# Kernel optimization log

Hardware: AMD Instinct MI355X
Metric: run time of the kernel (lower is better)

Reference implementation:

```python
import jax, jax.numpy as jnp
import numpy as np

# ---------------- irreps metadata: list of (mul, l, parity) ----------------
IR_A  = [(1, 0, 1)]                                        # '0e' input scalars
IR_B  = [(10,0,1),(10,0,-1),(10,0,1),(5,1,1),(5,1,-1)]     # Gate input, dim 60
IR_C  = [(10,0,1),(10,0,-1),(5,1,1),(5,1,-1)]              # Gate output, dim 50
IR_D  = [(1,0,-1),(6,0,1)]                                 # '0o + 6x0e', dim 7
IR_SH = [(1,0,1),(1,1,-1)]                                 # '0e + 1o'
CONVS = [(IR_A,IR_B),(IR_C,IR_B),(IR_C,IR_B),(IR_C,IR_B),(IR_C,IR_D)]
R_BASIS  = 2
DIAMETER = 5.0   # source used 1.5 -> degenerate 1^3 kernel; enlarged to exercise the steerable conv
STEP     = 1.0

def irdim(ir):
    return sum(m*(2*l+1) for m,l,_ in ir)

def irslices(ir):
    out, o = [], 0
    for m,l,_ in ir:
        d = m*(2*l+1); out.append(slice(o,o+d)); o += d
    return out

# normalized Clebsch-Gordan (wigner3j * sqrt(2*l_out+1)) for l<=1
_eps = np.zeros((3,3,3))
for a,b,c in [(0,1,2),(1,2,0),(2,0,1)]:
    _eps[a,b,c] = 1.0; _eps[b,a,c] = -1.0
CG = {
    (0,0,0): np.ones((1,1,1)),
    (0,1,1): np.eye(3).reshape(1,3,3),
    (1,0,1): np.eye(3).reshape(3,1,3),
    (1,1,0): (np.eye(3)/np.sqrt(3.0)).reshape(3,3,1),
    (1,1,1): _eps/np.sqrt(2.0),
}

def tp_ins(ir1, iro):
    ins = []
    for i1,(m1,l1,p1) in enumerate(ir1):
        for i2,(m2,l2,p2) in enumerate(IR_SH):
            for io,(mo,lo,po) in enumerate(iro):
                if po == p1*p2 and abs(l1-l2) <= lo <= l1+l2:
                    ins.append((i1,i2,io))
    return ins

def tp_numel(ir1, iro):
    return sum(R_BASIS*ir1[i1][0]*IR_SH[i2][0]*iro[io][0] for i1,i2,io in tp_ins(ir1,iro))

def lin_ins(ir1, iro):
    return [(i,j) for i,(m1,l1,p1) in enumerate(ir1)
                  for j,(m2,l2,p2) in enumerate(iro) if l1==l2 and p1==p2]

def lin_numel(ir1, iro):
    return sum(ir1[i][0]*iro[j][0] for i,j in lin_ins(ir1,iro))

def _lattice_features():
    # lattice offsets, smooth_finite radial basis (with cutoff) and SH ('0e+1o', component norm)
    r = DIAMETER/2.0
    s = int(np.floor(r/STEP))
    c = np.arange(-s, s+1, dtype=np.float64)*STEP
    lat = np.stack(np.meshgrid(c, c, c, indexing='ij'), -1)            # [K,K,K,3]
    d = np.linalg.norm(lat, axis=-1)
    vals = np.linspace(0.0, r, R_BASIS+2)[1:-1]
    step = vals[1]-vals[0]
    diff = (d[...,None]-vals)/step
    sus = lambda t: np.where(t>0, np.exp(-1.0/np.where(t>0, t, 1.0)), 0.0)
    emb = 1.14136*np.exp(2.0)*sus(diff+1.0)*sus(1.0-diff)              # [K,K,K,R]
    unit = lat/np.maximum(d, 1e-9)[...,None]
    sh = np.concatenate([np.ones_like(d)[...,None],
                         np.sqrt(3.0)*unit[...,[1,2,0]]], -1)          # [K,K,K,4], e3nn (y,z,x) order
    return jnp.asarray(emb, jnp.float32), jnp.asarray(sh, jnp.float32)

EMB, SH = _lattice_features()

def build_kernel(ir_in, ir_out, tw, lw):
    sin, sout, ssh = irslices(ir_in), irslices(ir_out), irslices(IR_SH)
    K = EMB.shape[0]
    k = jnp.zeros((K, K, K, irdim(ir_in), irdim(ir_out)), jnp.float32)
    off = 0
    for i1,i2,io in tp_ins(ir_in, ir_out):
        m1,l1,_ = ir_in[i1]; m2,l2,_ = IR_SH[i2]; mo,lo,_ = ir_out[io]
        n = R_BASIS*m1*m2*mo
        w = tw[off:off+n].reshape(R_BASIS, m1, mo); off += n           # m2 == 1 for SH
        cg = jnp.asarray(CG[(l1,l2,lo)], jnp.float32)
        alpha = 1.0/np.sqrt(m1*m2*R_BASIS)
        shseg = SH[..., ssh[i2]]                                       # [K,K,K,2l2+1]
        blk = alpha*jnp.einsum('xyzr,ruw,xyzj,ijk->xyzuiwk', EMB, w, shseg, cg)
        k = k.at[:,:,:, sin[i1], sout[io]].add(
            blk.reshape(K, K, K, m1*(2*l1+1), mo*(2*lo+1)))
    # self-connection Linear at the kernel center (radial basis vanishes at r=0)
    M = jnp.zeros((irdim(ir_in), irdim(ir_out)), jnp.float32)
    off = 0
    for i,j in lin_ins(ir_in, ir_out):
        m1,l1,_ = ir_in[i]; mo,_,_ = ir_out[j]
        w = lw[off:off+m1*mo].reshape(m1, mo); off += m1*mo
        eye = jnp.eye(2*l1+1, dtype=jnp.float32)
        blk = (1.0/np.sqrt(m1))*jnp.einsum('uw,ik->uiwk', w, eye)
        M = M.at[sin[i], sout[j]].add(blk.reshape(m1*(2*l1+1), mo*(2*l1+1)))
    cc = K//2
    return k.at[cc, cc, cc].set(M)

def equiv_conv(x, k):
    return jax.lax.conv_general_dilated(x, k, (1,1,1), 'SAME',
        dimension_numbers=('NXYZC', 'XYZIO', 'NXYZC'))

def gate(y):
    # Gate('10x0e+10x0o', [gelu, tanh], '10x0e', [sigmoid], '5x1e+5x1o')
    s = jnp.concatenate([jax.nn.gelu(y[..., :10]), jnp.tanh(y[..., 10:20])], -1)
    g = jax.nn.sigmoid(y[..., 20:30])                                  # 10 gate scalars
    v = y[..., 30:60].reshape(y.shape[:-1]+(10,3))*g[..., None]        # gate 5x1e + 5x1o
    return jnp.concatenate([s, v.reshape(y.shape[:-1]+(30,))], -1)

def _forward(x, tws, lws):
    y = x
    for i,(a,b) in enumerate(CONVS):
        y = equiv_conv(y, build_kernel(a, b, tws[i], lws[i]))
        if i < len(CONVS)-1:
            y = gate(y)
    return jnp.sum(y, axis=(1, 2, 3))                                  # [B, 7]

def setup_inputs() -> dict:
    key = jax.random.key(0)
    ks = jax.random.split(key, 11)
    inp = {'x': jax.random.normal(ks[0], (2, 48, 48, 48, 1), jnp.float32)}
    for i,(a,b) in enumerate(CONVS):
        inp[f'tp_w{i}'] = jax.random.normal(ks[1+i], (tp_numel(a,b),), jnp.float32)
        inp[f'lin_w{i}'] = jax.random.normal(ks[6+i], (lin_numel(a,b),), jnp.float32)
    return inp

def reference(x, tp_w0, tp_w1, tp_w2, tp_w3, tp_w4,
              lin_w0, lin_w1, lin_w2, lin_w3, lin_w4):
    return _forward(x, [tp_w0, tp_w1, tp_w2, tp_w3, tp_w4],
                    [lin_w0, lin_w1, lin_w2, lin_w3, lin_w4])
```

## Files before the change

kernel.cpp:

```cpp
#include <hip/hip_runtime.h>
#include <hip/hip_bf16.h>
#include <math.h>


typedef __attribute__((ext_vector_type(8))) short bf16x8;
typedef __attribute__((ext_vector_type(4))) float f32x4;
typedef __attribute__((ext_vector_type(4))) unsigned int u32x4;

struct TpPath { int off, ci, co, m1, l1, i2, mo, lo; float alpha; };
struct LinPath { int off, ci, co, m1, l, mo; float norm; };

__device__ __constant__ TpPath g_tp[19] = {
  {0,  0,  0, 1, 0, 0, 10, 0, 0.70710678f},
  {20, 0, 20, 1, 0, 0, 10, 0, 0.70710678f},
  {40, 0, 45, 1, 0, 1,  5, 1, 0.70710678f},
  {0,    0,  0, 10, 0, 0, 10, 0, 0.22360680f},
  {200,  0, 20, 10, 0, 0, 10, 0, 0.22360680f},
  {400,  0, 45, 10, 0, 1,  5, 1, 0.22360680f},
  {500, 10, 10, 10, 0, 0, 10, 0, 0.22360680f},
  {700, 10, 30, 10, 0, 1,  5, 1, 0.22360680f},
  {800, 20, 30,  5, 1, 0,  5, 1, 0.31622777f},
  {850, 20, 10,  5, 1, 1, 10, 0, 0.31622777f},
  {950, 20, 45,  5, 1, 1,  5, 1, 0.31622777f},
  {1000,35, 45,  5, 1, 0,  5, 1, 0.31622777f},
  {1050,35,  0,  5, 1, 1, 10, 0, 0.31622777f},
  {1150,35, 20,  5, 1, 1, 10, 0, 0.31622777f},
  {1250,35, 30,  5, 1, 1,  5, 1, 0.31622777f},
  {0,    0, 1, 10, 0, 0, 6, 0, 0.22360680f},
  {120, 10, 0, 10, 0, 0, 1, 0, 0.22360680f},
  {140, 20, 0,  5, 1, 1, 1, 0, 0.31622777f},
  {150, 35, 1,  5, 1, 1, 6, 0, 0.31622777f},
};

__device__ __constant__ LinPath g_lin[9] = {
  {0,  0,  0, 1, 0, 10, 1.0f},
  {10, 0, 20, 1, 0, 10, 1.0f},
  {0,   0,  0, 10, 0, 10, 0.31622777f},
  {100, 0, 20, 10, 0, 10, 0.31622777f},
  {200,10, 10, 10, 0, 10, 0.31622777f},
  {300,20, 30,  5, 1,  5, 0.44721360f},
  {325,35, 45,  5, 1,  5, 0.44721360f},
  {0,  0, 1, 10, 0, 6, 0.31622777f},
  {60,10, 0, 10, 0, 1, 0.31622777f},
};

__device__ inline float sus_f(float t) { return t > 0.f ? __expf(-1.f / t) : 0.f; }

__global__ void build_tp_kernel(const float* __restrict__ tw, float* __restrict__ kbuf,
                                int CIN, int COUT, int path_base) {
  TpPath p = g_tp[path_base + blockIdx.x];
  const int dl1 = 2 * p.l1 + 1, dlo = 2 * p.lo + 1;
  const int du = p.m1 * dl1, dw = p.mo * dlo;
  const int total = 125 * du * dw;
  const float C0 = 1.14136f * expf(2.0f);
  for (int e = threadIdx.x; e < total; e += blockDim.x) {
    int xyz = e / (du * dw);
    int rem = e % (du * dw);
    int ui = rem / dw, wk = rem % dw;
    int u = ui / dl1, i = ui % dl1;
    int w = wk / dlo, kk = wk % dlo;
    int kx = xyz / 25, ky = (xyz / 5) % 5, kz = xyz % 5;
    float cx = (float)(kx - 2), cy = (float)(ky - 2), cz = (float)(kz - 2);
    float d = sqrtf(cx * cx + cy * cy + cz * cz);
    float t = 1.2f * d;
    float e0 = C0 * sus_f(t) * sus_f(2.f - t);
    float e1 = C0 * sus_f(t - 1.f) * sus_f(3.f - t);
    float radial = e0 * tw[p.off + (0 * p.m1 + u) * p.mo + w] +
                   e1 * tw[p.off + (1 * p.m1 + u) * p.mo + w];
    float invd = (d > 0.f) ? 1.f / d : 0.f;
    const float s3 = 1.7320508f;
    float sh1[3] = { s3 * cy * invd, s3 * cz * invd, s3 * cx * invd };
    float shfac;
    if (p.l1 == 0 && p.i2 == 0)      shfac = 1.f;
    else if (p.l1 == 0)              shfac = sh1[kk];
    else if (p.i2 == 0)              shfac = (i == kk) ? 1.f : 0.f;
    else if (p.lo == 0)              shfac = sh1[i] * 0.57735027f;
    else {
      if (i == kk) shfac = 0.f;
      else {
        int j = 3 - i - kk;
        float sgn = (j == (i + 1) % 3) ? 1.f : -1.f;
        shfac = sgn * sh1[j] * 0.70710678f;
      }
    }
    kbuf[(size_t)(xyz * CIN + p.ci + ui) * COUT + p.co + wk] = p.alpha * radial * shfac;
  }
}

__global__ void set_center_kernel(const float* __restrict__ lw, float* __restrict__ kbuf,
                                  int CIN, int COUT, int lin_base, int nlin) {
  for (int l = 0; l < nlin; l++) {
    LinPath q = g_lin[lin_base + l];
    int dl = 2 * q.l + 1;
    int tot = q.m1 * q.mo * dl;
    for (int e = threadIdx.x; e < tot; e += blockDim.x) {
      int u = e / (q.mo * dl);
      int r = e % (q.mo * dl);
      int w = r / dl, ii = r % dl;
      kbuf[(size_t)(62 * CIN + q.ci + u * dl + ii) * COUT + q.co + w * dl + ii] =
          q.norm * lw[q.off + u * q.mo + w];
    }
  }
}

__global__ void convert_w(const float* __restrict__ kbuf, unsigned short* __restrict__ kwbT,
                          int CIN, int COUT) {
  int idx = blockIdx.x * 256 + threadIdx.x;
  if (idx >= 125 * 64 * 64) return;
  int tap = idx >> 12, co = (idx >> 6) & 63, ci = idx & 63;
  float v = (ci < CIN && co < COUT) ? kbuf[((size_t)tap * CIN + ci) * COUT + co] : 0.f;
  __hip_bfloat16 h = __float2bfloat16(v);
  kwbT[idx] = *(unsigned short*)&h;
}

__global__ void build_w0(const float* __restrict__ k0, unsigned short* __restrict__ wb0L) {
  int idx = blockIdx.x * 256 + threadIdx.x;
  if (idx >= 5 * 2 * 64 * 32) return;
  int k = idx & 31, co = (idx >> 5) & 63, mf = (idx >> 11) & 1, dxi = idx >> 12;
  float v = 0.f;
  if (co < 60) {
    if (mf == 0) {
      int dy = k >> 3, dz = k & 7;
      if (dz < 5) v = k0[(size_t)(((dxi * 5 + dy) * 5 + dz)) * 60 + co];
    } else {
      int kg = k >> 3, dz = k & 7;
      if (kg == 0 && dz < 5) v = k0[(size_t)(((dxi * 5 + 4) * 5 + dz)) * 60 + co];
    }
  }
  __hip_bfloat16 h = __float2bfloat16(v);
  wb0L[idx] = *(unsigned short*)&h;
}

__device__ inline float gelu_f(float x) {
  float inner = 0.79788456f * (x + 0.044715f * x * x * x);
  return 0.5f * x * (1.f + tanhf(inner));
}
__device__ inline float sigm_f(float x) { return 1.f / (1.f + __expf(-x)); }

__device__ inline int eidx(int c, int z) {
  return c * 16 + ((((z >> 2) ^ (c & 3)) << 2) | (z & 3));
}
__device__ inline int oidx(int z, int p) { return z * 32 + (p ^ z); }
__device__ inline int uidx(int e) {
  return (e & ~31) | ((e & 31) ^ ((e >> 5) & 15));
}

__device__ inline void gate_tile(const float* my, unsigned int* myO, int z) {
#pragma unroll
  for (int p = 0; p < 25; p++) {
    float a0, a1;
    if (p < 5) {
      a0 = gelu_f(my[eidx(2 * p, z)]);
      a1 = gelu_f(my[eidx(2 * p + 1, z)]);
    } else if (p < 10) {
      a0 = tanhf(my[eidx(2 * p, z)]);
      a1 = tanhf(my[eidx(2 * p + 1, z)]);
    } else {
      int q0 = 2 * (p - 10), q1 = q0 + 1;
      a0 = my[eidx(30 + q0, z)] * sigm_f(my[eidx(20 + q0 / 3, z)]);
      a1 = my[eidx(30 + q1, z)] * sigm_f(my[eidx(20 + q1 / 3, z)]);
    }
    __hip_bfloat162 p2;
    p2.x = __float2bfloat16(a0);
    p2.y = __float2bfloat16(a1);
    myO[oidx(z, p)] = *(unsigned int*)&p2;
  }
#pragma unroll
  for (int p = 25; p < 32; p++) myO[oidx(z, p)] = 0u;
}

template <int NT>
__device__ inline void epilogue_gate(f32x4 (&acc)[3][NT], float* my,
                                     unsigned short* out_, int n, int x, int y,
                                     int l, int lm, int kg) {
  unsigned int* myO = (unsigned int*)(my + 1024);
#pragma unroll
  for (int zt = 0; zt < 3; zt++) {
#pragma unroll
    for (int nt = 0; nt < NT; nt++)
      *(f32x4*)(my + (lm + 16 * nt) * 16 + ((kg ^ (lm & 3)) << 2)) = acc[zt][nt];
    if (l < 16) gate_tile(my, myO, l);
    unsigned int* gout = (unsigned int*)out_ +
        ((size_t)(((n * 48 + x) * 48 + y) * 48 + 16 * zt)) * 32;
#pragma unroll 1
    for (int e = l; e < 512; e += 64) gout[e] = myO[uidx(e)];
  }
}

template <int CIN, int COUT, int MODE>
__global__ __launch_bounds__(512, 2)
void conv_mfma(const unsigned short* __restrict__ act, const short* __restrict__ kwbT,
               void* __restrict__ out_) {
  constexpr int NTH = (MODE == 0) ? 2 : 1;
  constexpr int KC = (CIN + 31) / 32;
  __shared__ __align__(16) unsigned int Albs[12 * 48 * 32];

  const int tid = threadIdx.x;
  const int l = tid & 63;
  const int w = tid >> 6;
  const int wp = w & 3;
  const int ch = w >> 2;
  const int lm = l & 15;
  const int kg = l >> 4;
  const int co_off = (MODE == 0) ? ch * 32 : 0;

  const int bid = blockIdx.x;
  const int yb = bid % 6;
  const int x = (bid / 6) % 48;
  const int n = bid / (6 * 48);

  int g_off[9]; bool g_ok[9]; int l_off[9];
#pragma unroll
  for (int i = 0; i < 9; i++) {
    int e = tid + i * 512;
    int yi = e / 384;
    int rem = e % 384;
    int zin = rem >> 3, u = rem & 7;
    int yin = 8 * yb + yi - 2;
    g_ok[i] = (yin >= 0) && (yin < 48);
    int yc = min(max(yin, 0), 47);
    g_off[i] = (yc * 48 + zin) * 64 + u * 8;
    l_off[i] = (yi * 48 + zin) * 32 + ((u ^ (zin & 7)) << 2);
  }

  f32x4 acc[2][3][NTH];
#pragma unroll
  for (int yy = 0; yy < 2; yy++)
#pragma unroll
    for (int zt = 0; zt < 3; zt++)
#pragma unroll
      for (int nt = 0; nt < NTH; nt++) acc[yy][zt][nt] = (f32x4){0.f, 0.f, 0.f, 0.f};

  u32x4 rg[9];
  const int xlo = max(x - 2, 0), xhi = min(x + 2, 47);

#define LOADP(xin_)                                                            \
  {                                                                            \
    const unsigned short* pb = act + (size_t)((n * 48 + (xin_)) * 2304) * 64;  \
    _Pragma("unroll")                                                          \
    for (int i = 0; i < 9; i++)                                                \
      rg[i] = g_ok[i] ? *(const u32x4*)(pb + g_off[i])                         \
                      : (u32x4){0u, 0u, 0u, 0u};                               \
  }

  LOADP(xlo);
#pragma unroll 1
  for (int xin = xlo; xin <= xhi; ++xin) {
    __syncthreads();
#pragma unroll
    for (int i = 0; i < 9; i++)
      *(u32x4*)((unsigned int*)Albs + l_off[i]) = rg[i];
    __syncthreads();
    if (xin < xhi) LOADP(xin + 1);

    if (MODE == 0 || w < 4) {
      const int dxi = xin - x + 2;
      const short* Albs_s = (const short*)Albs;
#pragma unroll 1
      for (int dy = 0; dy < 5; dy++) {
        const int tapbase = (dxi * 5 + dy) * 5;
#pragma unroll
        for (int dz = 0; dz < 5; dz++) {
          bf16x8 bfr[NTH * KC];
          {
            const short* wb_ = kwbT + ((size_t)(tapbase + dz) << 12) +
                               (co_off + lm) * 64 + kg * 8;
#pragma unroll
            for (int nt = 0; nt < NTH; nt++)
#pragma unroll
              for (int kc = 0; kc < KC; kc++)
                bfr[nt * KC + kc] = *(const bf16x8*)(wb_ + nt * 1024 + kc * 32);
          }
          bf16x8 afr[2][3][KC];
#pragma unroll
          for (int zt = 0; zt < 3; zt++) {
            const int zraw = 16 * zt + lm + dz - 2;
            const int zc = min(max(zraw, 0), 47);
            const bool zval = (zraw >= 0) && (zraw < 48);
#pragma unroll
            for (int yy = 0; yy < 2; yy++) {
              const int yrow = 2 * wp + yy + dy;
              const int rowoff = (yrow * 48 + zc) * 64;
#pragma unroll
              for (int kc = 0; kc < KC; kc++) {
                int u = (4 * kc + kg) ^ (zc & 7);
                bf16x8 v = *(const bf16x8*)(Albs_s + rowoff + u * 8);
                afr[yy][zt][kc] = zval ? v : (bf16x8)(short)0;
              }
            }
          }
#pragma unroll
          for (int yy = 0; yy < 2; yy++)
#pragma unroll
            for (int zt = 0; zt < 3; zt++)
#pragma unroll
              for (int nt = 0; nt < NTH; nt++)
#pragma unroll
                for (int kc = 0; kc < KC; kc++)
                  acc[yy][zt][nt] = __builtin_amdgcn_mfma_f32_16x16x32_bf16(
                      afr[yy][zt][kc], bfr[nt * KC + kc], acc[yy][zt][nt], 0, 0, 0);
        }
      }
    }
  }
#undef LOADP

  if constexpr (MODE == 0) {
    __syncthreads();
    float* base = (float*)Albs;
    int par = 0;
#pragma unroll
    for (int yy = 0; yy < 2; yy++) {
#pragma unroll
      for (int zt = 0; zt < 3; zt++) {
        float* my = base + par * 6144 + wp * 1536;
        unsigned int* myO = (unsigned int*)(my + 1024);
#pragma unroll
        for (int nt = 0; nt < NTH; nt++)
          *(f32x4*)(my + (co_off + lm + 16 * nt) * 16 + ((kg ^ (lm & 3)) << 2)) =
              acc[yy][zt][nt];
        __syncthreads();
        if (ch == 0 && l < 16) gate_tile(my, myO, l);
        __syncthreads();
        unsigned int* gout = (unsigned int*)out_ +
            ((size_t)(((n * 48 + x) * 48 + (8 * yb + 2 * wp + yy)) * 48 + 16 * zt)) * 32;
#pragma unroll
        for (int q = 0; q < 4; q++) {
          int e = ch * 256 + q * 64 + l;
          gout[e] = myO[uidx(e)];
        }
        par ^= 1;
      }
    }
  } else {
    if (w < 4) {
      float s = 0.f;
#pragma unroll
      for (int yy = 0; yy < 2; yy++)
#pragma unroll
        for (int zt = 0; zt < 3; zt++)
#pragma unroll
          for (int r = 0; r < 4; r++) s += acc[yy][zt][0][r];
      s += __shfl_xor(s, 16);
      s += __shfl_xor(s, 32);
      if (l < 7) atomicAdd(&((float*)out_)[n * 7 + l], s);
    }
  }
}

__global__ __launch_bounds__(256, 4)
void conv0_mfma(const float* __restrict__ in_, const short* __restrict__ wb0L,
                unsigned short* __restrict__ out_) {
  __shared__ float A0[8 * 72];
  __shared__ __align__(16) float outbuf0[4 * 1536];

  const int tid = threadIdx.x;
  const int l = tid & 63;
  const int w = tid >> 6;
  const int lm = l & 15;
  const int kg = l >> 4;
  const int yb = blockIdx.x % 12;
  const int x = (blockIdx.x / 12) % 48;
  const int n = blockIdx.x / (12 * 48);

  f32x4 acc[3][4];
#pragma unroll
  for (int zt = 0; zt < 3; zt++)
#pragma unroll
    for (int nt = 0; nt < 4; nt++) acc[zt][nt] = (f32x4){0.f, 0.f, 0.f, 0.f};

  for (int dxi = 0; dxi < 5; dxi++) {
    int xin = x + dxi - 2;
    if (xin < 0 || xin >= 48) continue;
    __syncthreads();
    for (int e = tid; e < 8 * 72; e += 256) {
      int yi = e / 72, zz = e % 72;
      int yin = 4 * yb + yi - 2, zin = zz - 2;
      A0[e] = (yin >= 0 && yin < 48 && zin >= 0 && zin < 48)
                  ? in_[(size_t)((n * 48 + xin) * 48 + yin) * 48 + zin] : 0.f;
    }
    __syncthreads();
#pragma unroll
    for (int mf = 0; mf < 2; mf++) {
      const short* wbp = wb0L + ((size_t)(dxi * 2 + mf) * 64 + lm) * 32 + kg * 8;
      bf16x8 bfr[4];
#pragma unroll
      for (int nt = 0; nt < 4; nt++) bfr[nt] = *(const bf16x8*)(wbp + nt * 16 * 32);
      const int row = mf ? (w + 4) : (w + kg);
#pragma unroll
      for (int zt = 0; zt < 3; zt++) {
        const float* ap = A0 + row * 72 + 16 * zt + lm;
        union { bf16x8 v; unsigned short s[8]; } af;
#pragma unroll
        for (int j = 0; j < 8; j++) {
          __hip_bfloat16 h = __float2bfloat16(ap[j]);
          af.s[j] = *(unsigned short*)&h;
        }
#pragma unroll
        for (int nt = 0; nt < 4; nt++)
          acc[zt][nt] = __builtin_amdgcn_mfma_f32_16x16x32_bf16(
              af.v, bfr[nt], acc[zt][nt], 0, 0, 0);
      }
    }
  }

  float* my = outbuf0 + w * 1536;
  epilogue_gate<4>(acc, my, out_, n, x, 4 * yb + w, l, lm, kg);
}

extern "C" void kernel_launch(void* const* d_in, const int* in_sizes, int n_in,
                              void* d_out, int out_size, void* d_ws, size_t ws_size,
                              hipStream_t stream) {
  const float* x   = (const float*)d_in[0];
  const float* tw0 = (const float*)d_in[1];
  const float* lw0 = (const float*)d_in[2];
  const float* tw1 = (const float*)d_in[3];
  const float* lw1 = (const float*)d_in[4];
  const float* tw2 = (const float*)d_in[5];
  const float* lw2 = (const float*)d_in[6];
  const float* tw3 = (const float*)d_in[7];
  const float* lw3 = (const float*)d_in[8];
  const float* tw4 = (const float*)d_in[9];
  const float* lw4 = (const float*)d_in[10];

  float* ws = (float*)d_ws;
  float* k0 = ws;
  float* k1 = k0 + 7500;
  float* k2 = k1 + 375000;
  float* k3 = k2 + 375000;
  float* k4 = k3 + 375000;
  unsigned short* actA = (unsigned short*)(ws + 1200000);
  unsigned short* actB = actA + 14155776;
  unsigned short* wb1 = (unsigned short*)(ws + 15360000);
  unsigned short* wb2 = wb1 + 512000;
  unsigned short* wb3 = wb2 + 512000;
  unsigned short* wb4 = wb3 + 512000;
  unsigned short* wb0L = wb4 + 512000;

  hipMemsetAsync(ws, 0, (size_t)1176250 * sizeof(float), stream);
  hipMemsetAsync(d_out, 0, (size_t)out_size * sizeof(float), stream);

  build_tp_kernel<<<3, 128, 0, stream>>>(tw0, k0, 1, 60, 0);
  build_tp_kernel<<<12, 128, 0, stream>>>(tw1, k1, 50, 60, 3);
  build_tp_kernel<<<12, 128, 0, stream>>>(tw2, k2, 50, 60, 3);
  build_tp_kernel<<<12, 128, 0, stream>>>(tw3, k3, 50, 60, 3);
  build_tp_kernel<<<4, 128, 0, stream>>>(tw4, k4, 50, 7, 15);
  set_center_kernel<<<1, 256, 0, stream>>>(lw0, k0, 1, 60, 0, 2);
  set_center_kernel<<<1, 256, 0, stream>>>(lw1, k1, 50, 60, 2, 5);
  set_center_kernel<<<1, 256, 0, stream>>>(lw2, k2, 50, 60, 2, 5);
  set_center_kernel<<<1, 256, 0, stream>>>(lw3, k3, 50, 60, 2, 5);
  set_center_kernel<<<1, 256, 0, stream>>>(lw4, k4, 50, 7, 7, 2);

  convert_w<<<2000, 256, 0, stream>>>(k1, wb1, 50, 60);
  convert_w<<<2000, 256, 0, stream>>>(k2, wb2, 50, 60);
  convert_w<<<2000, 256, 0, stream>>>(k3, wb3, 50, 60);
  convert_w<<<2000, 256, 0, stream>>>(k4, wb4, 50, 7);
  build_w0<<<80, 256, 0, stream>>>(k0, wb0L);

  const int grid0 = 2 * 48 * 12;
  const int grid  = 2 * 48 * 6;
  conv0_mfma<<<grid0, 256, 0, stream>>>(x, (const short*)wb0L, actA);
  conv_mfma<50, 60, 0><<<grid, 512, 0, stream>>>(actA, (const short*)wb1, actB);
  conv_mfma<50, 60, 0><<<grid, 512, 0, stream>>>(actB, (const short*)wb2, actA);
  conv_mfma<50, 60, 0><<<grid, 512, 0, stream>>>(actA, (const short*)wb3, actB);
  conv_mfma<50, 7, 1><<<grid, 512, 0, stream>>>(actB, (const short*)wb4, d_out);
}
```

Before: 1.987 ms.

## Restructure conv tiling: one y-row per wave, all output channels per wave

The conv kernel now uses 12 waves per block, each computing one y row across all output-channel tiles, instead of 8 waves splitting two y rows and output-channel halves. The block covers 12 y rows instead of 8, so the 4-row halo is amortised over more outputs and the grid shrinks. The MODE 1 path no longer idles half the waves. In exchange each wave does more weight loads per A fragment, the LDS tile grows, and register pressure rises under the 768-thread launch bound.

```diff
diff --git a/kernel.cpp b/kernel.cpp
--- a/kernel.cpp
+++ b/kernel.cpp
@@ -188,57 +188,52 @@
 }
 
 template <int CIN, int COUT, int MODE>
-__global__ __launch_bounds__(512, 2)
+__global__ __launch_bounds__(768, 3)
 void conv_mfma(const unsigned short* __restrict__ act, const short* __restrict__ kwbT,
                void* __restrict__ out_) {
-  constexpr int NTH = (MODE == 0) ? 2 : 1;
+  constexpr int NT = (COUT + 15) / 16;
   constexpr int KC = (CIN + 31) / 32;
-  __shared__ __align__(16) unsigned int Albs[12 * 48 * 32];
+  __shared__ __align__(16) unsigned int Albs[16 * 48 * 32];
 
   const int tid = threadIdx.x;
   const int l = tid & 63;
   const int w = tid >> 6;
-  const int wp = w & 3;
-  const int ch = w >> 2;
   const int lm = l & 15;
   const int kg = l >> 4;
-  const int co_off = (MODE == 0) ? ch * 32 : 0;
 
   const int bid = blockIdx.x;
-  const int yb = bid % 6;
-  const int x = (bid / 6) % 48;
-  const int n = bid / (6 * 48);
-
-  int g_off[9]; bool g_ok[9]; int l_off[9];
-#pragma unroll
-  for (int i = 0; i < 9; i++) {
-    int e = tid + i * 512;
+  const int yb = bid % 4;
+  const int x = (bid / 4) % 48;
+  const int n = bid / (4 * 48);
+
+  int g_off[8]; bool g_ok[8]; int l_off[8];
+#pragma unroll
+  for (int i = 0; i < 8; i++) {
+    int e = tid + i * 768;
     int yi = e / 384;
     int rem = e % 384;
     int zin = rem >> 3, u = rem & 7;
-    int yin = 8 * yb + yi - 2;
+    int yin = 12 * yb + yi - 2;
     g_ok[i] = (yin >= 0) && (yin < 48);
     int yc = min(max(yin, 0), 47);
     g_off[i] = (yc * 48 + zin) * 64 + u * 8;
     l_off[i] = (yi * 48 + zin) * 32 + ((u ^ (zin & 7)) << 2);
   }
 
-  f32x4 acc[2][3][NTH];
-#pragma unroll
-  for (int yy = 0; yy < 2; yy++)
-#pragma unroll
-    for (int zt = 0; zt < 3; zt++)
-#pragma unroll
-      for (int nt = 0; nt < NTH; nt++) acc[yy][zt][nt] = (f32x4){0.f, 0.f, 0.f, 0.f};
-
-  u32x4 rg[9];
+  f32x4 acc[3][NT];
+#pragma unroll
+  for (int zt = 0; zt < 3; zt++)
+#pragma unroll
+    for (int nt = 0; nt < NT; nt++) acc[zt][nt] = (f32x4){0.f, 0.f, 0.f, 0.f};
+
+  u32x4 rg[8];
   const int xlo = max(x - 2, 0), xhi = min(x + 2, 47);
 
 #define LOADP(xin_)                                                            \
   {                                                                            \
     const unsigned short* pb = act + (size_t)((n * 48 + (xin_)) * 2304) * 64;  \
     _Pragma("unroll")                                                          \
-    for (int i = 0; i < 9; i++)                                                \
+    for (int i = 0; i < 8; i++)                                                \
       rg[i] = g_ok[i] ? *(const u32x4*)(pb + g_off[i])                         \
                       : (u32x4){0u, 0u, 0u, 0u};                               \
   }
@@ -248,57 +243,46 @@
   for (int xin = xlo; xin <= xhi; ++xin) {
     __syncthreads();
 #pragma unroll
-    for (int i = 0; i < 9; i++)
+    for (int i = 0; i < 8; i++)
       *(u32x4*)((unsigned int*)Albs + l_off[i]) = rg[i];
     __syncthreads();
     if (xin < xhi) LOADP(xin + 1);
 
-    if (MODE == 0 || w < 4) {
-      const int dxi = xin - x + 2;
-      const short* Albs_s = (const short*)Albs;
+    const int dxi = xin - x + 2;
+    const short* Albs_s = (const short*)Albs;
 #pragma unroll 1
-      for (int dy = 0; dy < 5; dy++) {
-        const int tapbase = (dxi * 5 + dy) * 5;
-#pragma unroll
-        for (int dz = 0; dz < 5; dz++) {
-          bf16x8 bfr[NTH * KC];
-          {
-            const short* wb_ = kwbT + ((size_t)(tapbase + dz) << 12) +
-                               (co_off + lm) * 64 + kg * 8;
-#pragma unroll
-            for (int nt = 0; nt < NTH; nt++)
-#pragma unroll
-              for (int kc = 0; kc < KC; kc++)
-                bfr[nt * KC + kc] = *(const bf16x8*)(wb_ + nt * 1024 + kc * 32);
+    for (int dy = 0; dy < 5; dy++) {
+      const int yrow = w + dy;
+      const int tapbase = (dxi * 5 + dy) * 5;
+#pragma unroll
+      for (int dz = 0; dz < 5; dz++) {
+        bf16x8 afr[3][KC];
+#pragma unroll
+        for (int zt = 0; zt < 3; zt++) {
+          const int zraw = 16 * zt + lm + dz - 2;
+          const int zc = min(max(zraw, 0), 47);
+          const bool zval = (zraw >= 0) && (zraw < 48);
+          const int rowoff = (yrow * 48 + zc) * 64;
+#pragma unroll
+          for (int kc = 0; kc < KC; kc++) {
+            int u = (4 * kc + kg) ^ (zc & 7);
+            bf16x8 v = *(const bf16x8*)(Albs_s + rowoff + u * 8);
+            afr[zt][kc] = zval ? v : (bf16x8)(short)0;
           }
-          bf16x8 afr[2][3][KC];
-#pragma unroll
-          for (int zt = 0; zt < 3; zt++) {
-            const int zraw = 16 * zt + lm + dz - 2;
-            const int zc = min(max(zraw, 0), 47);
-            const bool zval = (zraw >= 0) && (zraw < 48);
-#pragma unroll
-            for (int yy = 0; yy < 2; yy++) {
-              const int yrow = 2 * wp + yy + dy;
-              const int rowoff = (yrow * 48 + zc) * 64;
-#pragma unroll
-              for (int kc = 0; kc < KC; kc++) {
-                int u = (4 * kc + kg) ^ (zc & 7);
-                bf16x8 v = *(const bf16x8*)(Albs_s + rowoff + u * 8);
-                afr[yy][zt][kc] = zval ? v : (bf16x8)(short)0;
-              }
-            }
-          }
-#pragma unroll
-          for (int yy = 0; yy < 2; yy++)
-#pragma unroll
-            for (int zt = 0; zt < 3; zt++)
-#pragma unroll
-              for (int nt = 0; nt < NTH; nt++)
-#pragma unroll
-                for (int kc = 0; kc < KC; kc++)
-                  acc[yy][zt][nt] = __builtin_amdgcn_mfma_f32_16x16x32_bf16(
-                      afr[yy][zt][kc], bfr[nt * KC + kc], acc[yy][zt][nt], 0, 0, 0);
+        }
+        const short* wb_ = kwbT + ((size_t)(tapbase + dz) << 12) + lm * 64 + kg * 8;
+#pragma unroll
+        for (int nt = 0; nt < NT; nt++) {
+          bf16x8 bfr[KC];
+#pragma unroll
+          for (int kc = 0; kc < KC; kc++)
+            bfr[kc] = *(const bf16x8*)(wb_ + nt * 1024 + kc * 32);
+#pragma unroll
+          for (int zt = 0; zt < 3; zt++)
+#pragma unroll
+            for (int kc = 0; kc < KC; kc++)
+              acc[zt][nt] = __builtin_amdgcn_mfma_f32_16x16x32_bf16(
+                  afr[zt][kc], bfr[kc], acc[zt][nt], 0, 0, 0);
         }
       }
     }
@@ -307,44 +291,18 @@
 
   if constexpr (MODE == 0) {
     __syncthreads();
-    float* base = (float*)Albs;
-    int par = 0;
-#pragma unroll
-    for (int yy = 0; yy < 2; yy++) {
-#pragma unroll
-      for (int zt = 0; zt < 3; zt++) {
-        float* my = base + par * 6144 + wp * 1536;
-        unsigned int* myO = (unsigned int*)(my + 1024);
-#pragma unroll
-        for (int nt = 0; nt < NTH; nt++)
-          *(f32x4*)(my + (co_off + lm + 16 * nt) * 16 + ((kg ^ (lm & 3)) << 2)) =
-              acc[yy][zt][nt];
-        __syncthreads();
-        if (ch == 0 && l < 16) gate_tile(my, myO, l);
-        __syncthreads();
-        unsigned int* gout = (unsigned int*)out_ +
-            ((size_t)(((n * 48 + x) * 48 + (8 * yb + 2 * wp + yy)) * 48 + 16 * zt)) * 32;
-#pragma unroll
-        for (int q = 0; q < 4; q++) {
-          int e = ch * 256 + q * 64 + l;
-          gout[e] = myO[uidx(e)];
-        }
-        par ^= 1;
-      }
-    }
+    float* my = (float*)Albs + w * 1536;
+    epilogue_gate<NT>(acc, my, (unsigned short*)out_, n, x, 12 * yb + w,
+                      l, lm, kg);
   } else {
-    if (w < 4) {
-      float s = 0.f;
-#pragma unroll
-      for (int yy = 0; yy < 2; yy++)
-#pragma unroll
-        for (int zt = 0; zt < 3; zt++)
-#pragma unroll
-          for (int r = 0; r < 4; r++) s += acc[yy][zt][0][r];
-      s += __shfl_xor(s, 16);
-      s += __shfl_xor(s, 32);
-      if (l < 7) atomicAdd(&((float*)out_)[n * 7 + l], s);
-    }
+    float s = 0.f;
+#pragma unroll
+    for (int zt = 0; zt < 3; zt++)
+#pragma unroll
+      for (int r = 0; r < 4; r++) s += acc[zt][0][r];
+    s += __shfl_xor(s, 16);
+    s += __shfl_xor(s, 32);
+    if (l < 7) atomicAdd(&((float*)out_)[n * 7 + l], s);
   }
 }
 
@@ -458,10 +416,10 @@
   build_w0<<<80, 256, 0, stream>>>(k0, wb0L);
 
   const int grid0 = 2 * 48 * 12;
-  const int grid  = 2 * 48 * 6;
+  const int grid  = 2 * 48 * 4;
   conv0_mfma<<<grid0, 256, 0, stream>>>(x, (const short*)wb0L, actA);
-  conv_mfma<50, 60, 0><<<grid, 512, 0, stream>>>(actA, (const short*)wb1, actB);
-  conv_mfma<50, 60, 0><<<grid, 512, 0, stream>>>(actB, (const short*)wb2, actA);
-  conv_mfma<50, 60, 0><<<grid, 512, 0, stream>>>(actA, (const short*)wb3, actB);
-  conv_mfma<50, 7, 1><<<grid, 512, 0, stream>>>(actB, (const short*)wb4, d_out);
-}
+  conv_mfma<50, 60, 0><<<grid, 768, 0, stream>>>(actA, (const short*)wb1, actB);
+  conv_mfma<50, 60, 0><<<grid, 768, 0, stream>>>(actB, (const short*)wb2, actA);
+  conv_mfma<50, 60, 0><<<grid, 768, 0, stream>>>(actA, (const short*)wb3, actB);
+  conv_mfma<50, 7, 1><<<grid, 768, 0, stream>>>(actB, (const short*)wb4, d_out);
+}
```

Result: slower. 3.011 ms (+51.6%).

## Load conv slabs directly to LDS and enlarge y-tile to twelve rows

Applied to the files above, without the earlier changes.

Replaces the register-staged prefetch of each x-slab (global to registers, then to LDS) with direct global_load_lds instructions. The source address is pre-swizzled, and out-of-range rows read from a zeroed guard buffer. The block grows to 12 waves covering 12 y-rows with a 16-row LDS halo tile, which cuts the halo overhead per output and the grid size. In exchange it drops the overlap of the next slab's load with compute, and it changes occupancy through the larger block and LDS footprint.

```diff
diff --git a/kernel.cpp b/kernel.cpp
--- a/kernel.cpp
+++ b/kernel.cpp
@@ -188,39 +188,39 @@
 }
 
 template <int CIN, int COUT, int MODE>
-__global__ __launch_bounds__(512, 2)
+__global__ __launch_bounds__(768, 3)
 void conv_mfma(const unsigned short* __restrict__ act, const short* __restrict__ kwbT,
-               void* __restrict__ out_) {
+               const unsigned short* __restrict__ zguard, void* __restrict__ out_) {
   constexpr int NTH = (MODE == 0) ? 2 : 1;
   constexpr int KC = (CIN + 31) / 32;
-  __shared__ __align__(16) unsigned int Albs[12 * 48 * 32];
+  __shared__ __align__(16) unsigned int Albs[16 * 48 * 32];
 
   const int tid = threadIdx.x;
   const int l = tid & 63;
   const int w = tid >> 6;
-  const int wp = w & 3;
-  const int ch = w >> 2;
+  const int wp = (MODE == 0) ? (w % 6) : w;
+  const int ch = (MODE == 0) ? (w / 6) : 0;
   const int lm = l & 15;
   const int kg = l >> 4;
-  const int co_off = (MODE == 0) ? ch * 32 : 0;
+  const int co_off = ch * 32;
 
   const int bid = blockIdx.x;
-  const int yb = bid % 6;
-  const int x = (bid / 6) % 48;
-  const int n = bid / (6 * 48);
-
-  int g_off[9]; bool g_ok[9]; int l_off[9];
-#pragma unroll
-  for (int i = 0; i < 9; i++) {
-    int e = tid + i * 512;
+  const int yb = bid % 4;
+  const int x = (bid / 4) % 48;
+  const int n = bid / (4 * 48);
+
+  int g_off[8]; bool g_ok[8];
+#pragma unroll
+  for (int i = 0; i < 8; i++) {
+    int e = tid + i * 768;
     int yi = e / 384;
     int rem = e % 384;
     int zin = rem >> 3, u = rem & 7;
-    int yin = 8 * yb + yi - 2;
+    int usrc = u ^ (zin & 7);
+    int yin = 12 * yb + yi - 2;
     g_ok[i] = (yin >= 0) && (yin < 48);
     int yc = min(max(yin, 0), 47);
-    g_off[i] = (yc * 48 + zin) * 64 + u * 8;
-    l_off[i] = (yi * 48 + zin) * 32 + ((u ^ (zin & 7)) << 2);
+    g_off[i] = (yc * 48 + zin) * 64 + usrc * 8;
   }
 
   f32x4 acc[2][3][NTH];
@@ -231,29 +231,23 @@
 #pragma unroll
       for (int nt = 0; nt < NTH; nt++) acc[yy][zt][nt] = (f32x4){0.f, 0.f, 0.f, 0.f};
 
-  u32x4 rg[9];
   const int xlo = max(x - 2, 0), xhi = min(x + 2, 47);
 
-#define LOADP(xin_)                                                            \
-  {                                                                            \
-    const unsigned short* pb = act + (size_t)((n * 48 + (xin_)) * 2304) * 64;  \
-    _Pragma("unroll")                                                          \
-    for (int i = 0; i < 9; i++)                                                \
-      rg[i] = g_ok[i] ? *(const u32x4*)(pb + g_off[i])                         \
-                      : (u32x4){0u, 0u, 0u, 0u};                               \
-  }
-
-  LOADP(xlo);
 #pragma unroll 1
   for (int xin = xlo; xin <= xhi; ++xin) {
     __syncthreads();
-#pragma unroll
-    for (int i = 0; i < 9; i++)
-      *(u32x4*)((unsigned int*)Albs + l_off[i]) = rg[i];
+    const unsigned short* pb = act + (size_t)((n * 48 + xin) * 2304) * 64;
+#pragma unroll
+    for (int i = 0; i < 8; i++) {
+      const unsigned short* src = g_ok[i] ? (pb + g_off[i]) : zguard;
+      __builtin_amdgcn_global_load_lds(
+          (const __attribute__((address_space(1))) unsigned int*)src,
+          (__attribute__((address_space(3))) unsigned int*)(Albs + (size_t)(i * 768 + w * 64) * 4),
+          16, 0, 0);
+    }
     __syncthreads();
-    if (xin < xhi) LOADP(xin + 1);
-
-    if (MODE == 0 || w < 4) {
+
+    if (MODE == 0 || w < 6) {
       const int dxi = xin - x + 2;
       const short* Albs_s = (const short*)Albs;
 #pragma unroll 1
@@ -303,7 +297,6 @@
       }
     }
   }
-#undef LOADP
 
   if constexpr (MODE == 0) {
     __syncthreads();
@@ -313,7 +306,7 @@
     for (int yy = 0; yy < 2; yy++) {
 #pragma unroll
       for (int zt = 0; zt < 3; zt++) {
-        float* my = base + par * 6144 + wp * 1536;
+        float* my = base + par * 9216 + wp * 1536;
         unsigned int* myO = (unsigned int*)(my + 1024);
 #pragma unroll
         for (int nt = 0; nt < NTH; nt++)
@@ -323,7 +316,7 @@
         if (ch == 0 && l < 16) gate_tile(my, myO, l);
         __syncthreads();
         unsigned int* gout = (unsigned int*)out_ +
-            ((size_t)(((n * 48 + x) * 48 + (8 * yb + 2 * wp + yy)) * 48 + 16 * zt)) * 32;
+            ((size_t)(((n * 48 + x) * 48 + (12 * yb + 2 * wp + yy)) * 48 + 16 * zt)) * 32;
 #pragma unroll
         for (int q = 0; q < 4; q++) {
           int e = ch * 256 + q * 64 + l;
@@ -333,7 +326,7 @@
       }
     }
   } else {
-    if (w < 4) {
+    if (w < 6) {
       float s = 0.f;
 #pragma unroll
       for (int yy = 0; yy < 2; yy++)
@@ -436,8 +429,10 @@
   unsigned short* wb3 = wb2 + 512000;
   unsigned short* wb4 = wb3 + 512000;
   unsigned short* wb0L = wb4 + 512000;
+  unsigned short* zg   = wb0L + 20480;
 
   hipMemsetAsync(ws, 0, (size_t)1176250 * sizeof(float), stream);
+  hipMemsetAsync(zg, 0, 64, stream);
   hipMemsetAsync(d_out, 0, (size_t)out_size * sizeof(float), stream);
 
   build_tp_kernel<<<3, 128, 0, stream>>>(tw0, k0, 1, 60, 0);
@@ -458,10 +453,10 @@
   build_w0<<<80, 256, 0, stream>>>(k0, wb0L);
 
   const int grid0 = 2 * 48 * 12;
-  const int grid  = 2 * 48 * 6;
+  const int grid  = 2 * 48 * 4;
   conv0_mfma<<<grid0, 256, 0, stream>>>(x, (const short*)wb0L, actA);
-  conv_mfma<50, 60, 0><<<grid, 512, 0, stream>>>(actA, (const short*)wb1, actB);
-  conv_mfma<50, 60, 0><<<grid, 512, 0, stream>>>(actB, (const short*)wb2, actA);
-  conv_mfma<50, 60, 0><<<grid, 512, 0, stream>>>(actA, (const short*)wb3, actB);
-  conv_mfma<50, 7, 1><<<grid, 512, 0, stream>>>(actB, (const short*)wb4, d_out);
-}
+  conv_mfma<50, 60, 0><<<grid, 768, 0, stream>>>(actA, (const short*)wb1, zg, actB);
+  conv_mfma<50, 60, 0><<<grid, 768, 0, stream>>>(actB, (const short*)wb2, zg, actA);
+  conv_mfma<50, 60, 0><<<grid, 768, 0, stream>>>(actA, (const short*)wb3, zg, actB);
+  conv_mfma<50, 7, 1><<<grid, 768, 0, stream>>>(actB, (const short*)wb4, zg, d_out);
+}
```

After: 1.930 ms. 1.03x faster.
